# Performance work log

Hardware: AMD Instinct MI355X
Metric: run time of the kernel (lower is better)

Reference implementation:

```python
import jax, jax.numpy as jnp
import numpy as np

N_SRC, N_DST, K, T = 16384, 8192, 16, 2
NODE_IN, EDGE_IN, TIME_D = 128, 64, 128
D_MODEL = NODE_IN + TIME_D + EDGE_IN  # 320
N_HEAD, D_K = 8, 64                   # d_k = d_v
HID = 128
LN_EPS = 1e-5


def setup_inputs() -> dict:
    key = jax.random.key(0)
    ks = jax.random.split(key, 10)
    std_qk = np.sqrt(2.0 / (D_MODEL + D_K)).astype(np.float32)
    return {
        "node_features": jax.random.normal(ks[0], (N_SRC, NODE_IN), jnp.float32),
        "edge_features": jax.random.normal(ks[1], (N_DST, K, T, EDGE_IN), jnp.float32),
        "delta_t": jax.random.uniform(ks[2], (N_DST, K, T), jnp.float32) * 100.0,
        "neigh_idx": jax.random.randint(ks[3], (N_DST, K), 0, N_SRC),
        "basis_freq": jnp.asarray(1.0 / 10 ** np.linspace(0, 9, TIME_D), jnp.float32),
        "phase": jnp.zeros((TIME_D,), jnp.float32),
        "w_qs": jax.random.normal(ks[4], (N_HEAD * D_K, D_MODEL), jnp.float32) * std_qk,
        "w_ks": jax.random.normal(ks[5], (N_HEAD * D_K, D_MODEL), jnp.float32) * std_qk,
        "w_vs": jax.random.normal(ks[6], (N_HEAD * D_K, D_MODEL), jnp.float32) * std_qk,
        "fc_w": jax.random.normal(ks[7], (D_MODEL, N_HEAD * D_K), jnp.float32) * 0.03,
        "fc_b": jnp.zeros((D_MODEL,), jnp.float32),
        "ln_g": jnp.ones((D_MODEL,), jnp.float32),
        "ln_b": jnp.zeros((D_MODEL,), jnp.float32),
        "node_w": jax.random.normal(ks[8], (HID, 2 * NODE_IN + TIME_D + EDGE_IN), jnp.float32) * 0.05,
        "node_b": jnp.zeros((HID,), jnp.float32),
    }


def reference(node_features, edge_features, delta_t, neigh_idx, basis_freq, phase,
              w_qs, w_ks, w_vs, fc_w, fc_b, ln_g, ln_b, node_w, node_b):
    h_dst = node_features[:N_DST]                                  # [N, NODE_IN]
    # message_func: per-edge time encoding + gather src feats + concat
    te = jnp.cos(delta_t[..., None] * basis_freq + phase)          # [N, K, T, TIME_D]
    h_nb = node_features[neigh_idx]                                # [N, K, NODE_IN] (irregular gather)
    h_nb = jnp.broadcast_to(h_nb[:, :, None, :], (N_DST, K, T, NODE_IN))
    m = jnp.concatenate([h_nb, edge_features, te], axis=-1)        # [N, K, T, D_MODEL]
    m = m.reshape(N_DST, K * T, D_MODEL)                           # mailbox kv
    # reduce_func query: [h_dst, zeros(edge_in), time_encode(0)=cos(phase)]
    t0 = jnp.broadcast_to(jnp.cos(phase), (N_DST, TIME_D))
    q = jnp.concatenate([h_dst, jnp.zeros((N_DST, EDGE_IN), h_dst.dtype), t0], axis=-1)  # [N, D_MODEL]
    # multi-head attention (len_q = 1)
    qh = (q @ w_qs.T).reshape(N_DST, N_HEAD, D_K)
    kh = (m @ w_ks.T).reshape(N_DST, K * T, N_HEAD, D_K)
    vh = (m @ w_vs.T).reshape(N_DST, K * T, N_HEAD, D_K)
    scores = jnp.einsum('nhd,nlhd->nhl', qh, kh) / np.float32(np.sqrt(D_K))
    attn = jax.nn.softmax(scores, axis=-1)
    ctx = jnp.einsum('nhl,nlhd->nhd', attn, vh).reshape(N_DST, N_HEAD * D_K)
    out = ctx @ fc_w.T + fc_b
    x = out + q                                                    # residual
    mu = x.mean(-1, keepdims=True)
    var = x.var(-1, keepdims=True)
    h_neigh = ln_g * (x - mu) * jax.lax.rsqrt(var + LN_EPS) + ln_b  # layer norm
    h = jnp.concatenate([h_dst, h_neigh], axis=-1)                 # [N, 2*NODE_IN+TIME_D+EDGE_IN]
    return jax.nn.relu(h @ node_w.T + node_b)                      # [N, HID]
```

## Files before the change

kernel.cpp:

```cpp
#include <hip/hip_runtime.h>
#include <math.h>

#define LNB      32
#define NODE_IN  128
#define EDGE_IN  64
#define TIME_D   128
#define D_MODEL  320
#define N_HEAD   8
#define D_K      64
#define NHD      512
#define HID      128
#define IN2      448
#define N_DSTN   8192

typedef __attribute__((ext_vector_type(8))) short bf16x8;
typedef __attribute__((ext_vector_type(4))) float f32x4;
#define MFMA16(a,b,c) __builtin_amdgcn_mfma_f32_16x16x32_bf16(a,b,c,0,0,0)

#define WS_QKM   0
#define WS_WQK   20971520
#define WS_WVF   21299200
#define WS_NWC   22118400
#define WS_F32   22175744
#define WS_X     22182784

#define F_C0     0
#define F_C0K    512
#define F_CC     3072
#define F_B2     3392

__device__ __forceinline__ unsigned short f2bf(float f) {
  __bf16 h = (__bf16)f;
  return __builtin_bit_cast(unsigned short, h);
}
__device__ __forceinline__ bf16x8 pack8(const float* v) {
  unsigned short b8[8];
  #pragma unroll
  for (int j = 0; j < 8; ++j) b8[j] = f2bf(v[j]);
  return *(const bf16x8*)b8;
}

#define GLDS(srcp, dstp) __builtin_amdgcn_global_load_lds(                     \
    (const __attribute__((address_space(1))) unsigned int*)(const void*)(srcp),\
    (__attribute__((address_space(3))) unsigned int*)(void*)(dstp), 16, 0, 0)

__global__ __launch_bounds__(256)
void prep1a(const float* __restrict__ nw, const float* __restrict__ lng,
            const float* __restrict__ fcb, const float* __restrict__ ph,
            unsigned short* __restrict__ ws)
{
  int i = blockIdx.x * 256 + threadIdx.x;
  unsigned short* nwc = ws + WS_NWC;
  float* f32r = (float*)(ws + WS_F32);
  if (i < 16384) {
    int o = i >> 7, k = i & 127;
    nwc[o * IN2 + k] = f2bf(nw[(size_t)o * IN2 + k]);
  } else if (i < 57344) {
    int j = i - 16384, o = j / 320, c = j - o * 320;
    nwc[o * IN2 + 128 + c] = f2bf(nw[(size_t)o * IN2 + 128 + c] * lng[c]);
  } else if (i < 57664) {
    int c = i - 57344;
    f32r[F_CC + c] = fcb[c] + (c >= 192 ? __cosf(ph[c - 192]) : 0.f);
  }
}

__global__ __launch_bounds__(256)
void prep1b(const float* __restrict__ wq, const float* __restrict__ ph,
            const float* __restrict__ nw, const float* __restrict__ lnb_,
            const float* __restrict__ nb, unsigned short* __restrict__ ws)
{
  float* f32r = (float*)(ws + WS_F32);
  int gw = (blockIdx.x * 256 + threadIdx.x) >> 6;
  int ln = threadIdx.x & 63;
  if (gw < 512) {
    float s = __cosf(ph[ln])      * wq[(size_t)gw * D_MODEL + 192 + ln]
            + __cosf(ph[ln + 64]) * wq[(size_t)gw * D_MODEL + 256 + ln];
    #pragma unroll
    for (int off = 32; off >= 1; off >>= 1) s += __shfl_xor(s, off);
    if (ln == 0) f32r[F_C0 + gw] = s;
  } else {
    int o = gw - 512;
    float s = 0.f;
    #pragma unroll
    for (int k = 0; k < 5; ++k) {
      int c = ln + 64 * k;
      s += nw[(size_t)o * IN2 + 128 + c] * lnb_[c];
    }
    #pragma unroll
    for (int off = 32; off >= 1; off >>= 1) s += __shfl_xor(s, off);
    if (ln == 0) f32r[F_B2 + o] = nb[o] + s;
  }
}

__global__ __launch_bounds__(256)
void prep_c0k(const float* __restrict__ wk, unsigned short* __restrict__ ws)
{
  float* f32r = (float*)(ws + WS_F32);
  int gw = (blockIdx.x * 256 + threadIdx.x) >> 6;
  int ln = threadIdx.x & 63;
  int h = gw / 320, d = gw - h * 320;
  float s = f32r[F_C0 + h * 64 + ln] * wk[(size_t)(h * 64 + ln) * D_MODEL + d];
  #pragma unroll
  for (int off = 32; off >= 1; off >>= 1) s += __shfl_xor(s, off);
  if (ln == 0) f32r[F_C0K + gw] = s;
}

__global__ __launch_bounds__(256)
void prep_wqk(const float* __restrict__ wq, const float* __restrict__ wk,
              unsigned short* __restrict__ ws)
{
  __shared__ float sQw[64 * 128];
  __shared__ float sKw[64 * 32];
  int h = blockIdx.x / 10, d0 = (blockIdx.x - h * 10) * 32;
  int tid = threadIdx.x;
  #pragma unroll 4
  for (int it = 0; it < 32; ++it) {
    int idx = it * 256 + tid;
    int r = idx >> 7, c = idx & 127;
    sQw[idx] = wq[(size_t)(h * 64 + r) * D_MODEL + c];
  }
  #pragma unroll
  for (int it = 0; it < 8; ++it) {
    int idx = it * 256 + tid;
    int r = idx >> 5, c = idx & 31;
    sKw[idx] = wk[(size_t)(h * 64 + r) * D_MODEL + d0 + c];
  }
  __syncthreads();
  int di = tid >> 3, k0 = (tid & 7) * 16;
  float acc[16] = {};
  for (int dk = 0; dk < 64; ++dk) {
    float w = sKw[dk * 32 + di];
    #pragma unroll
    for (int j = 0; j < 16; ++j) acc[j] += w * sQw[dk * 128 + k0 + j];
  }
  unsigned short* dst = ws + WS_WQK + (size_t)(h * 320 + d0 + di) * 128 + k0;
  #pragma unroll
  for (int j = 0; j < 16; ++j) dst[j] = f2bf(acc[j]);
}

__global__ __launch_bounds__(256)
void prep_wvf(const float* __restrict__ fcw, const float* __restrict__ wv,
              unsigned short* __restrict__ ws)
{
  __shared__ float sF[32 * 64];
  __shared__ float sW[64 * 32];
  int b = blockIdx.x;
  int h = b / 100, r2 = b - h * 100;
  int ct = r2 / 10;
  int c0 = ct * 32, d0 = (r2 - ct * 10) * 32;
  int tid = threadIdx.x;
  #pragma unroll
  for (int it = 0; it < 8; ++it) {
    int idx = it * 256 + tid;
    int i = idx >> 6, jj = idx & 63;
    sF[idx] = fcw[(size_t)(c0 + i) * NHD + h * 64 + jj];
  }
  #pragma unroll
  for (int it = 0; it < 8; ++it) {
    int idx = it * 256 + tid;
    int jj = idx >> 5, i = idx & 31;
    sW[idx] = wv[(size_t)(h * 64 + jj) * D_MODEL + d0 + i];
  }
  __syncthreads();
  int ci = tid >> 3, dj0 = (tid & 7) * 4;
  float acc[4] = {};
  for (int jj = 0; jj < 64; ++jj) {
    float f = sF[ci * 64 + jj];
    #pragma unroll
    for (int k = 0; k < 4; ++k) acc[k] += f * sW[jj * 32 + dj0 + k];
  }
  unsigned short* wvf = ws + WS_WVF;
  #pragma unroll
  for (int k = 0; k < 4; ++k)
    wvf[(size_t)(c0 + ci) * 2560 + (size_t)(d0 + dj0 + k) * 8 + h] = f2bf(acc[k]);
}

__global__ __launch_bounds__(256, 6)
void tgat_qk(const float* __restrict__ nf, const unsigned short* __restrict__ ws,
             unsigned short* __restrict__ qkm)
{
  __shared__ alignas(16) unsigned short sA[64 * 136];
  const int tid = threadIdx.x, wid = tid >> 6, lane = tid & 63, qd = lane >> 4, lm = lane & 15;
  const int mt_blk = blockIdx.x / 20, nt_blk = blockIdx.x - mt_blk * 20;
  const int n0 = mt_blk * 64, c0 = nt_blk * 128;
  const unsigned short* wqk = ws + WS_WQK;
  const float* f32r = (const float*)(ws + WS_F32);

  {
    int n = tid >> 2, k0 = (tid & 3) * 32;
    const float4* src = (const float4*)(nf + (size_t)(n0 + n) * NODE_IN + k0);
    #pragma unroll
    for (int q = 0; q < 4; ++q) {
      float4 f0 = src[2 * q], f1 = src[2 * q + 1];
      float v[8] = {f0.x, f0.y, f0.z, f0.w, f1.x, f1.y, f1.z, f1.w};
      *(bf16x8*)&sA[n * 136 + k0 + q * 8] = pack8(v);
    }
  }
  __syncthreads();

  f32x4 acc[2][4] = {};
  for (int kt = 0; kt < 4; ++kt) {
    bf16x8 a[4];
    #pragma unroll
    for (int mt = 0; mt < 4; ++mt)
      a[mt] = *(const bf16x8*)&sA[(mt * 16 + lm) * 136 + kt * 32 + qd * 8];
    #pragma unroll
    for (int t = 0; t < 2; ++t) {
      int cg = c0 + (2 * wid + t) * 16 + lm;
      bf16x8 b = *(const bf16x8*)&wqk[(size_t)cg * 128 + kt * 32 + qd * 8];
      #pragma unroll
      for (int mt = 0; mt < 4; ++mt) acc[t][mt] = MFMA16(a[mt], b, acc[t][mt]);
    }
  }
  #pragma unroll
  for (int t = 0; t < 2; ++t) {
    int cg = c0 + (2 * wid + t) * 16 + lm;
    float ck = f32r[F_C0K + cg];
    #pragma unroll
    for (int mt = 0; mt < 4; ++mt)
      #pragma unroll
      for (int r = 0; r < 4; ++r)
        qkm[(size_t)(n0 + mt * 16 + qd * 4 + r) * 2560 + cg] = f2bf(acc[t][mt][r] + ck);
  }
}

__global__ __launch_bounds__(256, 6)
void tgat_attn(const float* __restrict__ nf, const float* __restrict__ ef,
               const float* __restrict__ dtp, const int* __restrict__ nidx,
               const float* __restrict__ freq, const float* __restrict__ ph,
               unsigned short* __restrict__ qkm)
{
  __shared__ alignas(16) unsigned short sM[LNB * 328];
  __shared__ alignas(16) unsigned short sATT[16 * 40];

  const int tid = threadIdx.x;
  const int wid = tid >> 6, lane = tid & 63, qd = lane >> 4, lm = lane & 15;
  const int n = blockIdx.x;
  unsigned short* qn = qkm + (size_t)n * 2560;

  #pragma unroll 1
  for (int it = 0; it < 5; ++it) {
    int g = it * 256 + tid;
    int l = g & 31, dg = g >> 5;
    int d0 = dg * 8;
    float v[8];
    if (dg < 16) {
      int ni = nidx[n * 16 + (l >> 1)];
      const float4* src = (const float4*)(nf + (size_t)ni * NODE_IN + d0);
      float4 f0 = src[0], f1 = src[1];
      v[0]=f0.x; v[1]=f0.y; v[2]=f0.z; v[3]=f0.w; v[4]=f1.x; v[5]=f1.y; v[6]=f1.z; v[7]=f1.w;
    } else if (dg < 24) {
      const float4* src = (const float4*)(ef + ((size_t)n * LNB + l) * EDGE_IN + (d0 - NODE_IN));
      float4 f0 = src[0], f1 = src[1];
      v[0]=f0.x; v[1]=f0.y; v[2]=f0.z; v[3]=f0.w; v[4]=f1.x; v[5]=f1.y; v[6]=f1.z; v[7]=f1.w;
    } else {
      int dd = d0 - 192;
      float dt = dtp[(size_t)n * LNB + l];
      const float4* fq = (const float4*)(freq + dd);
      const float4* pp = (const float4*)(ph + dd);
      float4 q0 = fq[0], q1 = fq[1], p0 = pp[0], p1 = pp[1];
      v[0] = __cosf(dt * q0.x + p0.x); v[1] = __cosf(dt * q0.y + p0.y);
      v[2] = __cosf(dt * q0.z + p0.z); v[3] = __cosf(dt * q0.w + p0.w);
      v[4] = __cosf(dt * q1.x + p1.x); v[5] = __cosf(dt * q1.y + p1.y);
      v[6] = __cosf(dt * q1.z + p1.z); v[7] = __cosf(dt * q1.w + p1.w);
    }
    *(bf16x8*)&sM[l * 328 + d0] = pack8(v);
  }

  bf16x8 qfrag[10];
  if (wid == 0) {
    #pragma unroll
    for (int kt = 0; kt < 10; ++kt) {
      qfrag[kt] = (bf16x8){0,0,0,0,0,0,0,0};
      if (lm < 8) qfrag[kt] = *(const bf16x8*)&qn[lm * 320 + kt * 32 + qd * 8];
    }
  }
  __syncthreads();

  const int tbeg = (wid == 0) ? 0 : 2 + (wid - 1) * 6;
  const int tcnt = (wid == 0) ? 2 : 6;
  bf16x8 afr[6];

  if (wid == 0) {
    f32x4 acc0 = {}, acc1 = {};
    #pragma unroll
    for (int kt = 0; kt < 10; ++kt) {
      bf16x8 a0 = *(const bf16x8*)&sM[lm * 328 + kt * 32 + qd * 8];
      bf16x8 a1 = *(const bf16x8*)&sM[(16 + lm) * 328 + kt * 32 + qd * 8];
      acc0 = MFMA16(a0, qfrag[kt], acc0);
      acc1 = MFMA16(a1, qfrag[kt], acc1);
    }
    float s[8], e[8];
    #pragma unroll
    for (int r = 0; r < 4; ++r) { s[r] = acc0[r] * 0.125f; s[4 + r] = acc1[r] * 0.125f; }
    float mx = s[0];
    #pragma unroll
    for (int i = 1; i < 8; ++i) mx = fmaxf(mx, s[i]);
    mx = fmaxf(mx, __shfl_xor(mx, 16));
    mx = fmaxf(mx, __shfl_xor(mx, 32));
    float sum = 0.f;
    #pragma unroll
    for (int i = 0; i < 8; ++i) { e[i] = __expf(s[i] - mx); sum += e[i]; }
    sum += __shfl_xor(sum, 16);
    sum += __shfl_xor(sum, 32);
    float inv = 1.f / sum;
    #pragma unroll
    for (int i = 0; i < 8; ++i) {
      int l = (i < 4) ? (qd * 4 + i) : (16 + qd * 4 + (i - 4));
      sATT[lm * 40 + l] = f2bf(e[i] * inv);
    }
  } else {
    #pragma unroll
    for (int u = 0; u < 6; ++u) {
      int d = (tbeg + u) * 16 + lm;
      unsigned short a8[8];
      #pragma unroll
      for (int j = 0; j < 8; ++j) a8[j] = sM[(qd * 8 + j) * 328 + d];
      afr[u] = *(const bf16x8*)a8;
    }
  }
  __syncthreads();

  if (wid == 0) {
    #pragma unroll
    for (int u = 0; u < 2; ++u) {
      int d = u * 16 + lm;
      unsigned short a8[8];
      #pragma unroll
      for (int j = 0; j < 8; ++j) a8[j] = sM[(qd * 8 + j) * 328 + d];
      afr[u] = *(const bf16x8*)a8;
    }
  }
  bf16x8 batt = *(const bf16x8*)&sATT[lm * 40 + qd * 8];
  #pragma unroll
  for (int u = 0; u < 6; ++u) {
    if (u < tcnt) {
      int dtile = tbeg + u;
      f32x4 acc = {};
      acc = MFMA16(afr[u], batt, acc);
      if (lm < 8) {
        #pragma unroll
        for (int r = 0; r < 4; ++r)
          qn[(dtile * 16 + qd * 4 + r) * 8 + lm] = f2bf(acc[r]);
      }
    }
  }
}

__global__ __launch_bounds__(512, 1)
void tgat_xgemm(const unsigned short* __restrict__ ws,
                const unsigned short* __restrict__ qkm, float* __restrict__ xacc)
{
  __shared__ alignas(16) unsigned short sA[2][128 * 128];
  __shared__ alignas(16) unsigned short sB[2][80 * 128];
  const int tid = threadIdx.x, wid = tid >> 6, lane = tid & 63;
  const int qd = lane >> 4, lm = lane & 15;
  const int xcd = blockIdx.x & 7, j = blockIdx.x >> 3;
  const int nb = j & 3, mb = xcd + 8 * (j >> 2);
  const int n0 = mb * 128, c0 = nb * 80;
  const unsigned short* wvf = ws + WS_WVF;

  const int rhi = lane >> 4, blo = lane & 15;

  #define STAGE(kc, buf) {                                                     \
    for (int ri = wid; ri < 52; ri += 8) {                                     \
      if (ri < 32) {                                                           \
        int r = ri * 4 + rhi;                                                  \
        int blk = blo ^ (r & 7);                                               \
        GLDS(qkm + (size_t)(n0 + r) * 2560 + (kc) * 128 + blk * 8,             \
             &sA[buf][ri * 512]);                                              \
      } else {                                                                 \
        int jb = ri - 32;                                                      \
        int r = jb * 4 + rhi;                                                  \
        int blk = blo ^ (r & 7);                                               \
        GLDS(wvf + (size_t)(c0 + r) * 2560 + (kc) * 128 + blk * 8,             \
             &sB[buf][jb * 512]);                                              \
      }                                                                        \
    } }

  f32x4 acc[5] = {};
  STAGE(0, 0);
  __syncthreads();

  for (int c = 0; c < 20; ++c) {
    if (c < 19) STAGE(c + 1, (c + 1) & 1);
    const unsigned short* Ab = sA[c & 1];
    const unsigned short* Bb = sB[c & 1];
    const int s = lm & 7;
    #pragma unroll
    for (int kt = 0; kt < 4; ++kt) {
      const int blk = ((kt << 2) | qd) ^ s;
      bf16x8 a = *(const bf16x8*)&Ab[(wid * 16 + lm) * 128 + blk * 8];
      #pragma unroll
      for (int u = 0; u < 5; ++u) {
        bf16x8 b = *(const bf16x8*)&Bb[(u * 16 + lm) * 128 + blk * 8];
        acc[u] = MFMA16(a, b, acc[u]);
      }
    }
    __syncthreads();
  }

  #pragma unroll
  for (int u = 0; u < 5; ++u)
    #pragma unroll
    for (int r = 0; r < 4; ++r)
      xacc[(size_t)(n0 + wid * 16 + qd * 4 + r) * 320 + c0 + u * 16 + lm] = acc[u][r];
  #undef STAGE
}

__global__ __launch_bounds__(256, 4)
void tgat_post2(const float* __restrict__ nf, const unsigned short* __restrict__ ws,
                const float* __restrict__ xacc, float* __restrict__ out)
{
  __shared__ alignas(16) unsigned short sQb[16 * 136];
  __shared__ alignas(16) unsigned short sXb[16 * 328];
  const int tid = threadIdx.x, wid = tid >> 6, lane = tid & 63, qd = lane >> 4, lm = lane & 15;
  const int n0 = blockIdx.x * 16;
  const unsigned short* nwc = ws + WS_NWC;
  const float* f32r = (const float*)(ws + WS_F32);

  {
    int nn = tid >> 4, kk = (tid & 15) * 8;
    const float4* src = (const float4*)(nf + (size_t)(n0 + nn) * NODE_IN + kk);
    float4 f0 = src[0], f1 = src[1];
    float v8[8] = {f0.x, f0.y, f0.z, f0.w, f1.x, f1.y, f1.z, f1.w};
    *(bf16x8*)&sQb[nn * 136 + kk] = pack8(v8);
  }
  const int rr = tid >> 4, cl = tid & 15;
  float v[20], s1 = 0.f, s2 = 0.f;
  #pragma unroll
  for (int u = 0; u < 20; ++u) {
    int c = u * 16 + cl;
    float x = xacc[(size_t)(n0 + rr) * 320 + c] + f32r[F_CC + c];
    if (c < 128) x += nf[(size_t)(n0 + rr) * NODE_IN + c];
    v[u] = x; s1 += x; s2 += x * x;
  }
  #pragma unroll
  for (int off = 8; off >= 1; off >>= 1) { s1 += __shfl_xor(s1, off); s2 += __shfl_xor(s2, off); }
  float mean = s1 * (1.f / D_MODEL);
  float var  = s2 * (1.f / D_MODEL) - mean * mean;
  float rstd = rsqrtf(var + 1e-5f);
  #pragma unroll
  for (int u = 0; u < 20; ++u) {
    int c = u * 16 + cl;
    sXb[rr * 328 + c] = f2bf((v[u] - mean) * rstd);
  }
  __syncthreads();

  #pragma unroll
  for (int t = 0; t < 2; ++t) {
    int o = (wid * 2 + t) * 16 + lm;
    f32x4 acc = {};
    for (int kt = 0; kt < 14; ++kt) {
      bf16x8 a;
      if (kt < 4) a = *(const bf16x8*)&sQb[lm * 136 + kt * 32 + qd * 8];
      else        a = *(const bf16x8*)&sXb[lm * 328 + (kt - 4) * 32 + qd * 8];
      bf16x8 b = *(const bf16x8*)&nwc[(size_t)o * IN2 + kt * 32 + qd * 8];
      acc = MFMA16(a, b, acc);
    }
    float bz = f32r[F_B2 + o];
    #pragma unroll
    for (int r = 0; r < 4; ++r)
      out[(size_t)(n0 + qd * 4 + r) * HID + o] = fmaxf(acc[r] + bz, 0.f);
  }
}

extern "C" void kernel_launch(void* const* d_in, const int* in_sizes, int n_in,
                              void* d_out, int out_size, void* d_ws, size_t ws_size,
                              hipStream_t stream) {
  const float* nf   = (const float*)d_in[0];
  const float* ef   = (const float*)d_in[1];
  const float* dtp  = (const float*)d_in[2];
  const int*   nidx = (const int*)  d_in[3];
  const float* freq = (const float*)d_in[4];
  const float* ph   = (const float*)d_in[5];
  const float* wq   = (const float*)d_in[6];
  const float* wk   = (const float*)d_in[7];
  const float* wv   = (const float*)d_in[8];
  const float* fcw  = (const float*)d_in[9];
  const float* fcb  = (const float*)d_in[10];
  const float* lng  = (const float*)d_in[11];
  const float* lnb_ = (const float*)d_in[12];
  const float* nw   = (const float*)d_in[13];
  const float* nb   = (const float*)d_in[14];
  float* out = (float*)d_out;
  unsigned short* ws = (unsigned short*)d_ws;
  unsigned short* qkm = ws + WS_QKM;
  float* xacc = (float*)(ws + WS_X);

  prep1a  <<<226, 256, 0, stream>>>(nw, lng, fcb, ph, ws);
  prep1b  <<<160, 256, 0, stream>>>(wq, ph, nw, lnb_, nb, ws);
  prep_c0k<<<640, 256, 0, stream>>>(wk, ws);
  prep_wqk<<<80,  256, 0, stream>>>(wq, wk, ws);
  prep_wvf<<<800, 256, 0, stream>>>(fcw, wv, ws);
  tgat_qk   <<<2560, 256, 0, stream>>>(nf, ws, qkm);
  tgat_attn <<<8192, 256, 0, stream>>>(nf, ef, dtp, nidx, freq, ph, qkm);
  tgat_xgemm<<<256,  512, 0, stream>>>(ws, qkm, xacc);
  tgat_post2<<<512,  256, 0, stream>>>(nf, ws, xacc, out);
}
```

Measured before the change: 253.8 us.

## Merge prep kernels into one launch and XOR-swizzle attention LDS tile

Folds four weight-preparation kernels into a single prep_all launch that dispatches on block index, cutting launch count. The tgat_attn shared-memory mailbox tile gets an XOR swizzle on columns, applied consistently to writes, row-fragment reads and the column-wise transposed reads, to reduce LDS bank conflicts. The occupancy hint for tgat_attn rises from 6 to 7 waves, which may force register pressure or spills. The merged prep kernel now reserves 40KB of shared memory for every block, including the simple elementwise ones, which can lower that kernel's occupancy.

Result: faster. 243.9 us (-3.9%).

```diff
diff --git a/kernel.cpp b/kernel.cpp
--- a/kernel.cpp
+++ b/kernel.cpp
@@ -45,50 +45,110 @@
     (__attribute__((address_space(3))) unsigned int*)(void*)(dstp), 16, 0, 0)
 
 __global__ __launch_bounds__(256)
-void prep1a(const float* __restrict__ nw, const float* __restrict__ lng,
-            const float* __restrict__ fcb, const float* __restrict__ ph,
-            unsigned short* __restrict__ ws)
-{
-  int i = blockIdx.x * 256 + threadIdx.x;
+void prep_all(const float* __restrict__ nw, const float* __restrict__ lng,
+              const float* __restrict__ fcb, const float* __restrict__ ph,
+              const float* __restrict__ wq, const float* __restrict__ lnb_,
+              const float* __restrict__ nb, const float* __restrict__ wk,
+              const float* __restrict__ fcw, const float* __restrict__ wv,
+              unsigned short* __restrict__ ws)
+{
+  __shared__ float smem[10240];
+  const int b = blockIdx.x, tid = threadIdx.x;
   unsigned short* nwc = ws + WS_NWC;
   float* f32r = (float*)(ws + WS_F32);
-  if (i < 16384) {
-    int o = i >> 7, k = i & 127;
-    nwc[o * IN2 + k] = f2bf(nw[(size_t)o * IN2 + k]);
-  } else if (i < 57344) {
-    int j = i - 16384, o = j / 320, c = j - o * 320;
-    nwc[o * IN2 + 128 + c] = f2bf(nw[(size_t)o * IN2 + 128 + c] * lng[c]);
-  } else if (i < 57664) {
-    int c = i - 57344;
-    f32r[F_CC + c] = fcb[c] + (c >= 192 ? __cosf(ph[c - 192]) : 0.f);
-  }
-}
-
-__global__ __launch_bounds__(256)
-void prep1b(const float* __restrict__ wq, const float* __restrict__ ph,
-            const float* __restrict__ nw, const float* __restrict__ lnb_,
-            const float* __restrict__ nb, unsigned short* __restrict__ ws)
-{
-  float* f32r = (float*)(ws + WS_F32);
-  int gw = (blockIdx.x * 256 + threadIdx.x) >> 6;
-  int ln = threadIdx.x & 63;
-  if (gw < 512) {
-    float s = __cosf(ph[ln])      * wq[(size_t)gw * D_MODEL + 192 + ln]
-            + __cosf(ph[ln + 64]) * wq[(size_t)gw * D_MODEL + 256 + ln];
-    #pragma unroll
-    for (int off = 32; off >= 1; off >>= 1) s += __shfl_xor(s, off);
-    if (ln == 0) f32r[F_C0 + gw] = s;
+
+  if (b < 226) {
+    int i = b * 256 + tid;
+    if (i < 16384) {
+      int o = i >> 7, k = i & 127;
+      nwc[o * IN2 + k] = f2bf(nw[(size_t)o * IN2 + k]);
+    } else if (i < 57344) {
+      int j = i - 16384, o = j / 320, c = j - o * 320;
+      nwc[o * IN2 + 128 + c] = f2bf(nw[(size_t)o * IN2 + 128 + c] * lng[c]);
+    } else if (i < 57664) {
+      int c = i - 57344;
+      f32r[F_CC + c] = fcb[c] + (c >= 192 ? __cosf(ph[c - 192]) : 0.f);
+    }
+  } else if (b < 386) {
+    int gw = ((b - 226) * 256 + tid) >> 6;
+    int ln = tid & 63;
+    if (gw < 512) {
+      float s = __cosf(ph[ln])      * wq[(size_t)gw * D_MODEL + 192 + ln]
+              + __cosf(ph[ln + 64]) * wq[(size_t)gw * D_MODEL + 256 + ln];
+      #pragma unroll
+      for (int off = 32; off >= 1; off >>= 1) s += __shfl_xor(s, off);
+      if (ln == 0) f32r[F_C0 + gw] = s;
+    } else {
+      int o = gw - 512;
+      float s = 0.f;
+      #pragma unroll
+      for (int k = 0; k < 5; ++k) {
+        int c = ln + 64 * k;
+        s += nw[(size_t)o * IN2 + 128 + c] * lnb_[c];
+      }
+      #pragma unroll
+      for (int off = 32; off >= 1; off >>= 1) s += __shfl_xor(s, off);
+      if (ln == 0) f32r[F_B2 + o] = nb[o] + s;
+    }
+  } else if (b < 466) {
+    float* sQw = smem;
+    float* sKw = smem + 8192;
+    int bw = b - 386;
+    int h = bw / 10, d0 = (bw - h * 10) * 32;
+    #pragma unroll 4
+    for (int it = 0; it < 32; ++it) {
+      int idx = it * 256 + tid;
+      int r = idx >> 7, c = idx & 127;
+      sQw[idx] = wq[(size_t)(h * 64 + r) * D_MODEL + c];
+    }
+    #pragma unroll
+    for (int it = 0; it < 8; ++it) {
+      int idx = it * 256 + tid;
+      int r = idx >> 5, c = idx & 31;
+      sKw[idx] = wk[(size_t)(h * 64 + r) * D_MODEL + d0 + c];
+    }
+    __syncthreads();
+    int di = tid >> 3, k0 = (tid & 7) * 16;
+    float acc[16] = {};
+    for (int dk = 0; dk < 64; ++dk) {
+      float w = sKw[dk * 32 + di];
+      #pragma unroll
+      for (int j = 0; j < 16; ++j) acc[j] += w * sQw[dk * 128 + k0 + j];
+    }
+    unsigned short* dst = ws + WS_WQK + (size_t)(h * 320 + d0 + di) * 128 + k0;
+    #pragma unroll
+    for (int j = 0; j < 16; ++j) dst[j] = f2bf(acc[j]);
   } else {
-    int o = gw - 512;
-    float s = 0.f;
-    #pragma unroll
-    for (int k = 0; k < 5; ++k) {
-      int c = ln + 64 * k;
-      s += nw[(size_t)o * IN2 + 128 + c] * lnb_[c];
-    }
-    #pragma unroll
-    for (int off = 32; off >= 1; off >>= 1) s += __shfl_xor(s, off);
-    if (ln == 0) f32r[F_B2 + o] = nb[o] + s;
+    float* sF = smem;
+    float* sW = smem + 2048;
+    int bb = b - 466;
+    int h = bb / 100, r2 = bb - h * 100;
+    int ct = r2 / 10;
+    int c0 = ct * 32, d0 = (r2 - ct * 10) * 32;
+    #pragma unroll
+    for (int it = 0; it < 8; ++it) {
+      int idx = it * 256 + tid;
+      int i = idx >> 6, jj = idx & 63;
+      sF[idx] = fcw[(size_t)(c0 + i) * NHD + h * 64 + jj];
+    }
+    #pragma unroll
+    for (int it = 0; it < 8; ++it) {
+      int idx = it * 256 + tid;
+      int jj = idx >> 5, i = idx & 31;
+      sW[idx] = wv[(size_t)(h * 64 + jj) * D_MODEL + d0 + i];
+    }
+    __syncthreads();
+    int ci = tid >> 3, dj0 = (tid & 7) * 4;
+    float acc[4] = {};
+    for (int jj = 0; jj < 64; ++jj) {
+      float f = sF[ci * 64 + jj];
+      #pragma unroll
+      for (int k = 0; k < 4; ++k) acc[k] += f * sW[jj * 32 + dj0 + k];
+    }
+    unsigned short* wvf = ws + WS_WVF;
+    #pragma unroll
+    for (int k = 0; k < 4; ++k)
+      wvf[(size_t)(c0 + ci) * 2560 + (size_t)(d0 + dj0 + k) * 8 + h] = f2bf(acc[k]);
   }
 }
 
@@ -103,76 +163,6 @@
   #pragma unroll
   for (int off = 32; off >= 1; off >>= 1) s += __shfl_xor(s, off);
   if (ln == 0) f32r[F_C0K + gw] = s;
-}
-
-__global__ __launch_bounds__(256)
-void prep_wqk(const float* __restrict__ wq, const float* __restrict__ wk,
-              unsigned short* __restrict__ ws)
-{
-  __shared__ float sQw[64 * 128];
-  __shared__ float sKw[64 * 32];
-  int h = blockIdx.x / 10, d0 = (blockIdx.x - h * 10) * 32;
-  int tid = threadIdx.x;
-  #pragma unroll 4
-  for (int it = 0; it < 32; ++it) {
-    int idx = it * 256 + tid;
-    int r = idx >> 7, c = idx & 127;
-    sQw[idx] = wq[(size_t)(h * 64 + r) * D_MODEL + c];
-  }
-  #pragma unroll
-  for (int it = 0; it < 8; ++it) {
-    int idx = it * 256 + tid;
-    int r = idx >> 5, c = idx & 31;
-    sKw[idx] = wk[(size_t)(h * 64 + r) * D_MODEL + d0 + c];
-  }
-  __syncthreads();
-  int di = tid >> 3, k0 = (tid & 7) * 16;
-  float acc[16] = {};
-  for (int dk = 0; dk < 64; ++dk) {
-    float w = sKw[dk * 32 + di];
-    #pragma unroll
-    for (int j = 0; j < 16; ++j) acc[j] += w * sQw[dk * 128 + k0 + j];
-  }
-  unsigned short* dst = ws + WS_WQK + (size_t)(h * 320 + d0 + di) * 128 + k0;
-  #pragma unroll
-  for (int j = 0; j < 16; ++j) dst[j] = f2bf(acc[j]);
-}
-
-__global__ __launch_bounds__(256)
-void prep_wvf(const float* __restrict__ fcw, const float* __restrict__ wv,
-              unsigned short* __restrict__ ws)
-{
-  __shared__ float sF[32 * 64];
-  __shared__ float sW[64 * 32];
-  int b = blockIdx.x;
-  int h = b / 100, r2 = b - h * 100;
-  int ct = r2 / 10;
-  int c0 = ct * 32, d0 = (r2 - ct * 10) * 32;
-  int tid = threadIdx.x;
-  #pragma unroll
-  for (int it = 0; it < 8; ++it) {
-    int idx = it * 256 + tid;
-    int i = idx >> 6, jj = idx & 63;
-    sF[idx] = fcw[(size_t)(c0 + i) * NHD + h * 64 + jj];
-  }
-  #pragma unroll
-  for (int it = 0; it < 8; ++it) {
-    int idx = it * 256 + tid;
-    int jj = idx >> 5, i = idx & 31;
-    sW[idx] = wv[(size_t)(h * 64 + jj) * D_MODEL + d0 + i];
-  }
-  __syncthreads();
-  int ci = tid >> 3, dj0 = (tid & 7) * 4;
-  float acc[4] = {};
-  for (int jj = 0; jj < 64; ++jj) {
-    float f = sF[ci * 64 + jj];
-    #pragma unroll
-    for (int k = 0; k < 4; ++k) acc[k] += f * sW[jj * 32 + dj0 + k];
-  }
-  unsigned short* wvf = ws + WS_WVF;
-  #pragma unroll
-  for (int k = 0; k < 4; ++k)
-    wvf[(size_t)(c0 + ci) * 2560 + (size_t)(d0 + dj0 + k) * 8 + h] = f2bf(acc[k]);
 }
 
 __global__ __launch_bounds__(256, 6)
@@ -224,7 +214,7 @@
   }
 }
 
-__global__ __launch_bounds__(256, 6)
+__global__ __launch_bounds__(256, 7)
 void tgat_attn(const float* __restrict__ nf, const float* __restrict__ ef,
                const float* __restrict__ dtp, const int* __restrict__ nidx,
                const float* __restrict__ freq, const float* __restrict__ ph,
@@ -264,7 +254,7 @@
       v[4] = __cosf(dt * q1.x + p1.x); v[5] = __cosf(dt * q1.y + p1.y);
       v[6] = __cosf(dt * q1.z + p1.z); v[7] = __cosf(dt * q1.w + p1.w);
     }
-    *(bf16x8*)&sM[l * 328 + d0] = pack8(v);
+    *(bf16x8*)&sM[l * 328 + (d0 ^ ((l & 24) << 1))] = pack8(v);
   }
 
   bf16x8 qfrag[10];
@@ -282,11 +272,13 @@
   bf16x8 afr[6];
 
   if (wid == 0) {
+    const int xa = (lm & 8) << 1;
+    const int xb = 32 + xa;
     f32x4 acc0 = {}, acc1 = {};
     #pragma unroll
     for (int kt = 0; kt < 10; ++kt) {
-      bf16x8 a0 = *(const bf16x8*)&sM[lm * 328 + kt * 32 + qd * 8];
-      bf16x8 a1 = *(const bf16x8*)&sM[(16 + lm) * 328 + kt * 32 + qd * 8];
+      bf16x8 a0 = *(const bf16x8*)&sM[lm * 328 + ((kt * 32 + qd * 8) ^ xa)];
+      bf16x8 a1 = *(const bf16x8*)&sM[(16 + lm) * 328 + ((kt * 32 + qd * 8) ^ xb)];
       acc0 = MFMA16(a0, qfrag[kt], acc0);
       acc1 = MFMA16(a1, qfrag[kt], acc1);
     }
@@ -312,10 +304,10 @@
   } else {
     #pragma unroll
     for (int u = 0; u < 6; ++u) {
-      int d = (tbeg + u) * 16 + lm;
+      int dc = ((tbeg + u) * 16 + lm) ^ (qd << 4);
       unsigned short a8[8];
       #pragma unroll
-      for (int j = 0; j < 8; ++j) a8[j] = sM[(qd * 8 + j) * 328 + d];
+      for (int j = 0; j < 8; ++j) a8[j] = sM[(qd * 8 + j) * 328 + dc];
       afr[u] = *(const bf16x8*)a8;
     }
   }
@@ -324,10 +316,10 @@
   if (wid == 0) {
     #pragma unroll
     for (int u = 0; u < 2; ++u) {
-      int d = u * 16 + lm;
+      int dc = (u * 16 + lm) ^ (qd << 4);
       unsigned short a8[8];
       #pragma unroll
-      for (int j = 0; j < 8; ++j) a8[j] = sM[(qd * 8 + j) * 328 + d];
+      for (int j = 0; j < 8; ++j) a8[j] = sM[(qd * 8 + j) * 328 + dc];
       afr[u] = *(const bf16x8*)a8;
     }
   }
@@ -488,11 +480,8 @@
   unsigned short* qkm = ws + WS_QKM;
   float* xacc = (float*)(ws + WS_X);
 
-  prep1a  <<<226, 256, 0, stream>>>(nw, lng, fcb, ph, ws);
-  prep1b  <<<160, 256, 0, stream>>>(wq, ph, nw, lnb_, nb, ws);
+  prep_all<<<1266, 256, 0, stream>>>(nw, lng, fcb, ph, wq, lnb_, nb, wk, fcw, wv, ws);
   prep_c0k<<<640, 256, 0, stream>>>(wk, ws);
-  prep_wqk<<<80,  256, 0, stream>>>(wq, wk, ws);
-  prep_wvf<<<800, 256, 0, stream>>>(fcw, wv, ws);
   tgat_qk   <<<2560, 256, 0, stream>>>(nf, ws, qkm);
   tgat_attn <<<8192, 256, 0, stream>>>(nf, ef, dtp, nidx, freq, ph, qkm);
   tgat_xgemm<<<256,  512, 0, stream>>>(ws, qkm, xacc);
```
